# Performance work log

Hardware: AMD Instinct MI355X
Metric: run time of the kernel (lower is better)

## Reference

```python
import jax, jax.numpy as jnp
import numpy as np

N_EMBD = 1024
N_HEAD = 16
HEAD_DIM = N_EMBD // N_HEAD


def setup_inputs() -> dict:
    key = jax.random.key(0)
    kx, kq, kk, kv, ko = jax.random.split(key, 5)
    B, T, C = 2, 2048, N_EMBD
    s = 1.0 / np.sqrt(C)
    return {
        "x": jax.random.normal(kx, (B, T, C), dtype=jnp.float32),
        "Wq": jax.random.normal(kq, (C, C), dtype=jnp.float32) * s,
        "Wk": jax.random.normal(kk, (C, C), dtype=jnp.float32) * s,
        "Wv": jax.random.normal(kv, (C, C), dtype=jnp.float32) * s,
        "Wo": jax.random.normal(ko, (C, C), dtype=jnp.float32) * s,
    }


def reference(x, Wq, Wk, Wv, Wo):
    B, T, C = x.shape
    H, D = N_HEAD, HEAD_DIM
    # projections (torch Linear: y = x @ W^T)
    q = (x @ Wq.T).reshape(B, T, H, D).transpose(0, 2, 1, 3)  # [B,H,T,D]
    k = (x @ Wk.T).reshape(B, T, H, D).transpose(0, 2, 1, 3)
    v = (x @ Wv.T).reshape(B, T, H, D).transpose(0, 2, 1, 3)
    scale = 1.0 / np.sqrt(D).astype(np.float32)
    scores = jnp.einsum("bhqd,bhkd->bhqk", q, k) * scale  # [B,H,T,T]
    causal = jnp.tril(jnp.ones((T, T), dtype=bool))
    scores = jnp.where(causal, scores, -jnp.inf)
    attn = jax.nn.softmax(scores, axis=-1)
    y = jnp.einsum("bhqk,bhkd->bhqd", attn, v)  # [B,H,T,D]
    y = y.transpose(0, 2, 1, 3).reshape(B, T, C)
    return y @ Wo.T
```

## Files before the change

kernel.cpp:

```cpp
#include <hip/hip_runtime.h>
#include <hip/hip_bf16.h>
#include <math.h>

#define SEQ   2048
#define CDIM  1024
#define NH    16
#define HD    64

typedef __attribute__((ext_vector_type(8))) short bf16x8;
typedef __attribute__((ext_vector_type(4))) float f32x4;
typedef __attribute__((ext_vector_type(4))) short short4v;

__device__ __forceinline__ short f2bf(float f) {
  return (short)__builtin_bit_cast(unsigned short, __float2bfloat16(f));
}

__device__ __forceinline__ void glds16(const short* g, short* l) {
  __builtin_amdgcn_global_load_lds(
      (const __attribute__((address_space(1))) unsigned int*)g,
      (__attribute__((address_space(3))) unsigned int*)l, 16, 0, 0);
}

__global__ void cvt_kernel(const float* __restrict__ src, short* __restrict__ dst, int n4) {
  int i = blockIdx.x * blockDim.x + threadIdx.x;
  if (i >= n4) return;
  float4 v = reinterpret_cast<const float4*>(src)[i];
  short4v o;
  o.x = f2bf(v.x); o.y = f2bf(v.y); o.z = f2bf(v.z); o.w = f2bf(v.w);
  reinterpret_cast<short4v*>(dst)[i] = o;
}

template<int MODE>
__global__ __launch_bounds__(256)
void gemm_bt(const short* __restrict__ A,
             const short* __restrict__ W0, const short* __restrict__ W1, const short* __restrict__ W2,
             short* __restrict__ ob0, short* __restrict__ ob1, short* __restrict__ ob2,
             float* __restrict__ of)
{
  constexpr int K = CDIM;
  const int z = (MODE == 0) ? blockIdx.z : 0;
  const short* W;
  short* outb = nullptr;
  if (MODE == 0) {
    W    = (z == 0) ? W0  : (z == 1) ? W1  : W2;
    outb = (z == 0) ? ob0 : (z == 1) ? ob1 : ob2;
  } else {
    W = W0;
  }
  const int m0 = blockIdx.y * 128;
  const int n0 = blockIdx.x * 128;

  __shared__ __align__(16) short As[128 * 32];
  __shared__ __align__(16) short Bs[128 * 32];

  const int tid  = threadIdx.x;
  const int lane = tid & 63;
  const int wid  = tid >> 6;
  const int wr   = wid >> 1;
  const int wc   = wid & 1;
  const int rl   = lane & 15;
  const int g    = lane >> 4;

  f32x4 acc[4][4];
#pragma unroll
  for (int i = 0; i < 4; ++i)
#pragma unroll
    for (int j = 0; j < 4; ++j)
      acc[i][j] = (f32x4){0.f, 0.f, 0.f, 0.f};

  const int lrow = lane >> 2;
  const int lcol = (lane & 3) * 8;
  const int arow = wid * 32 + lrow;

  for (int kt = 0; kt < K / 32; ++kt) {
    const int k0 = kt * 32;
    glds16(&A[(size_t)(m0 + arow) * K + k0 + lcol],      &As[(wid * 32) * 32]);
    glds16(&A[(size_t)(m0 + arow + 16) * K + k0 + lcol], &As[(wid * 32 + 16) * 32]);
    glds16(&W[(size_t)(n0 + arow) * K + k0 + lcol],      &Bs[(wid * 32) * 32]);
    glds16(&W[(size_t)(n0 + arow + 16) * K + k0 + lcol], &Bs[(wid * 32 + 16) * 32]);
    __syncthreads();

    bf16x8 af[4], bfr[4];
#pragma unroll
    for (int mi = 0; mi < 4; ++mi)
      af[mi] = *(const bf16x8*)&As[(wr * 64 + mi * 16 + rl) * 32 + g * 8];
#pragma unroll
    for (int nj = 0; nj < 4; ++nj)
      bfr[nj] = *(const bf16x8*)&Bs[(wc * 64 + nj * 16 + rl) * 32 + g * 8];
#pragma unroll
    for (int mi = 0; mi < 4; ++mi)
#pragma unroll
      for (int nj = 0; nj < 4; ++nj)
        acc[mi][nj] = __builtin_amdgcn_mfma_f32_16x16x32_bf16(af[mi], bfr[nj], acc[mi][nj], 0, 0, 0);
    __syncthreads();
  }

#pragma unroll
  for (int mi = 0; mi < 4; ++mi) {
#pragma unroll
    for (int nj = 0; nj < 4; ++nj) {
      const int gmb = m0 + wr * 64 + mi * 16 + g * 4;
      const int gn  = n0 + wc * 64 + nj * 16 + rl;
      if (MODE == 0 && z == 2) {
        short4v pk;
#pragma unroll
        for (int r = 0; r < 4; ++r) pk[r] = f2bf(acc[mi][nj][r]);
        const int b = gmb >> 11, t = gmb & 2047;
        const int h = gn >> 6,  d = gn & 63;
        *(short4v*)&outb[(((size_t)(b * NH + h)) * HD + d) * SEQ + t] = pk;
      } else {
#pragma unroll
        for (int r = 0; r < 4; ++r) {
          const int gm = gmb + r;
          const float val = acc[mi][nj][r];
          if (MODE == 0) {
            const int b = gm >> 11, t = gm & 2047;
            const int h = gn >> 6,  d = gn & 63;
            outb[(((size_t)(b * NH + h)) * SEQ + t) * HD + d] = f2bf(val);
          } else {
            of[(size_t)gm * CDIM + gn] = val;
          }
        }
      }
    }
  }
}

__global__ __launch_bounds__(256)
void attn_kernel(const short* __restrict__ q, const short* __restrict__ k,
                 const short* __restrict__ vt, short* __restrict__ yb)
{
  const int bh  = blockIdx.y;
  const int pp  = blockIdx.x;
  const int jA  = pp;
  const int jB  = 31 - pp;
  const int tid = threadIdx.x;
  const int lane = tid & 63;
  const int wid  = tid >> 6;
  const int rl   = lane & 15;
  const int g    = lane >> 4;

  const short* Qp = q  + (size_t)bh * SEQ * HD;
  const short* Kp = k  + (size_t)bh * SEQ * HD;
  const short* Vp = vt + (size_t)bh * HD * SEQ;

  __shared__ short Ks[64 * 72];
  __shared__ short Vs[64 * 72];
  __shared__ short Ps[4][2][16 * 72];

  const int q0A = jA * 64 + wid * 16;
  const int q0B = jB * 64 + wid * 16;

  bf16x8 qfA[2], qfB[2];
#pragma unroll
  for (int ds = 0; ds < 2; ++ds) {
    qfA[ds] = *(const bf16x8*)&Qp[(size_t)(q0A + rl) * HD + ds * 32 + g * 8];
    qfB[ds] = *(const bf16x8*)&Qp[(size_t)(q0B + rl) * HD + ds * 32 + g * 8];
  }

  f32x4 accA[4], accB[4];
  float mA[4], lA[4], mB[4], lB[4];
#pragma unroll
  for (int r = 0; r < 4; ++r) { mA[r] = -INFINITY; lA[r] = 0.f; mB[r] = -INFINITY; lB[r] = 0.f; }
#pragma unroll
  for (int nt = 0; nt < 4; ++nt) { accA[nt] = (f32x4){0,0,0,0}; accB[nt] = (f32x4){0,0,0,0}; }

  const float scale = 0.125f;
  const int srow = tid >> 3;
  const int scol = (tid & 7) * 8;

  auto process = [&](bf16x8 (&qf)[2], f32x4 (&acc)[4], float (&m_run)[4], float (&l_run)[4],
                     bool diag, short* PsW) {
    f32x4 s_[4];
#pragma unroll
    for (int ct = 0; ct < 4; ++ct) s_[ct] = (f32x4){0, 0, 0, 0};
    __builtin_amdgcn_s_setprio(1);
#pragma unroll
    for (int ct = 0; ct < 4; ++ct)
#pragma unroll
      for (int ds = 0; ds < 2; ++ds) {
        bf16x8 kf = *(const bf16x8*)&Ks[(ct * 16 + rl) * 72 + ds * 32 + g * 8];
        s_[ct] = __builtin_amdgcn_mfma_f32_16x16x32_bf16(qf[ds], kf, s_[ct], 0, 0, 0);
      }
    __builtin_amdgcn_s_setprio(0);

    float pm[4] = {-INFINITY, -INFINITY, -INFINITY, -INFINITY};
#pragma unroll
    for (int ct = 0; ct < 4; ++ct)
#pragma unroll
      for (int r = 0; r < 4; ++r) {
        float sv = s_[ct][r] * scale;
        if (diag) {
          const int lq = wid * 16 + g * 4 + r;
          const int lk = ct * 16 + rl;
          sv = (lk <= lq) ? sv : -INFINITY;
        }
        s_[ct][r] = sv;
        pm[r] = fmaxf(pm[r], sv);
      }

    bool need = false;
#pragma unroll
    for (int r = 0; r < 4; ++r) need = need || (pm[r] > m_run[r]);
    if (__any((int)need)) {
#pragma unroll
      for (int r = 0; r < 4; ++r) {
        pm[r] = fmaxf(pm[r], __shfl_xor(pm[r], 1));
        pm[r] = fmaxf(pm[r], __shfl_xor(pm[r], 2));
        pm[r] = fmaxf(pm[r], __shfl_xor(pm[r], 4));
        pm[r] = fmaxf(pm[r], __shfl_xor(pm[r], 8));
        const float mnew = fmaxf(m_run[r], pm[r]);
        const float f = __expf(m_run[r] - mnew);
        m_run[r] = mnew;
        l_run[r] *= f;
#pragma unroll
        for (int nt = 0; nt < 4; ++nt) acc[nt][r] *= f;
      }
    }

#pragma unroll
    for (int ct = 0; ct < 4; ++ct) {
      const int c = ct * 16 + rl;
#pragma unroll
      for (int r = 0; r < 4; ++r) {
        const float p = __expf(s_[ct][r] - m_run[r]);
        l_run[r] += p;
        PsW[(g * 4 + r) * 72 + c] = f2bf(p);
      }
    }

    __builtin_amdgcn_s_setprio(1);
#pragma unroll
    for (int ks = 0; ks < 2; ++ks) {
      bf16x8 pf = *(const bf16x8*)&PsW[rl * 72 + ks * 32 + g * 8];
#pragma unroll
      for (int nt = 0; nt < 4; ++nt) {
        bf16x8 vf = *(const bf16x8*)&Vs[(nt * 16 + rl) * 72 + ks * 32 + g * 8];
        acc[nt] = __builtin_amdgcn_mfma_f32_16x16x32_bf16(pf, vf, acc[nt], 0, 0, 0);
      }
    }
    __builtin_amdgcn_s_setprio(0);
  };

  auto epilogue = [&](f32x4 (&acc)[4], float (&l_run)[4], int q0w) {
    const int b = bh >> 4, h = bh & 15;
#pragma unroll
    for (int r = 0; r < 4; ++r) {
      float lr = l_run[r];
      lr += __shfl_xor(lr, 1);
      lr += __shfl_xor(lr, 2);
      lr += __shfl_xor(lr, 4);
      lr += __shfl_xor(lr, 8);
      const float inv = 1.0f / lr;
      const int qq = q0w + g * 4 + r;
#pragma unroll
      for (int nt = 0; nt < 4; ++nt)
        yb[((size_t)b * SEQ + qq) * CDIM + h * HD + nt * 16 + rl] = f2bf(acc[nt][r] * inv);
    }
  };

  bf16x8 k0 = *(const bf16x8*)&Kp[(size_t)srow * HD + scol];
  bf16x8 k1 = *(const bf16x8*)&Kp[(size_t)(srow + 32) * HD + scol];
  bf16x8 v0 = *(const bf16x8*)&Vp[(size_t)srow * SEQ + scol];
  bf16x8 v1 = *(const bf16x8*)&Vp[(size_t)(srow + 32) * SEQ + scol];

  for (int t = 0; t <= jB; ++t) {
    __syncthreads();
    *(bf16x8*)&Ks[srow * 72 + scol]        = k0;
    *(bf16x8*)&Ks[(srow + 32) * 72 + scol] = k1;
    *(bf16x8*)&Vs[srow * 72 + scol]        = v0;
    *(bf16x8*)&Vs[(srow + 32) * 72 + scol] = v1;
    __syncthreads();

    if (t < jB) {
      const int kn = (t + 1) * 64;
      k0 = *(const bf16x8*)&Kp[(size_t)(kn + srow) * HD + scol];
      k1 = *(const bf16x8*)&Kp[(size_t)(kn + srow + 32) * HD + scol];
      v0 = *(const bf16x8*)&Vp[(size_t)srow * SEQ + kn + scol];
      v1 = *(const bf16x8*)&Vp[(size_t)(srow + 32) * SEQ + kn + scol];
    }

    process(qfB, accB, mB, lB, t == jB, &Ps[wid][0][0]);
    if (t <= jA)
      process(qfA, accA, mA, lA, t == jA, &Ps[wid][1][0]);
  }

  epilogue(accB, lB, q0B);
  epilogue(accA, lA, q0A);
}

extern "C" void kernel_launch(void* const* d_in, const int* in_sizes, int n_in,
                              void* d_out, int out_size, void* d_ws, size_t ws_size,
                              hipStream_t stream) {
  const float* x  = (const float*)d_in[0];
  const float* Wq = (const float*)d_in[1];
  const float* Wk = (const float*)d_in[2];
  const float* Wv = (const float*)d_in[3];
  const float* Wo = (const float*)d_in[4];
  float* out = (float*)d_out;

  char* ws = (char*)d_ws;
  short* xb  = (short*)(ws);
  short* Wqb = (short*)(ws + ((size_t)8  << 20));
  short* Wkb = (short*)(ws + ((size_t)10 << 20));
  short* Wvb = (short*)(ws + ((size_t)12 << 20));
  short* Wob = (short*)(ws + ((size_t)14 << 20));
  short* qb  = (short*)(ws + ((size_t)16 << 20));
  short* kbp = (short*)(ws + ((size_t)24 << 20));
  short* vtp = (short*)(ws + ((size_t)32 << 20));
  short* yb  = (short*)(ws + ((size_t)40 << 20));

  cvt_kernel<<<4096, 256, 0, stream>>>(x,  xb,  1048576);
  cvt_kernel<<<1024, 256, 0, stream>>>(Wq, Wqb, 262144);
  cvt_kernel<<<1024, 256, 0, stream>>>(Wk, Wkb, 262144);
  cvt_kernel<<<1024, 256, 0, stream>>>(Wv, Wvb, 262144);
  cvt_kernel<<<1024, 256, 0, stream>>>(Wo, Wob, 262144);

  gemm_bt<0><<<dim3(8, 32, 3), 256, 0, stream>>>(xb, Wqb, Wkb, Wvb, qb, kbp, vtp, nullptr);

  attn_kernel<<<dim3(16, 32), 256, 0, stream>>>(qb, kbp, vtp, yb);

  gemm_bt<1><<<dim3(8, 32, 1), 256, 0, stream>>>(yb, Wob, nullptr, nullptr,
                                                 nullptr, nullptr, nullptr, out);
}
```

Measured before the change: 137.8 us.

## Split attention into 32-row query tiles with per-wave pairing and exp2 softmax

The attention kernel now works on 32-row query tiles with twice as many blocks. Waves 0-1 take the late tile jB and waves 2-3 take the early tile jA, so each wave keeps one accumulator set instead of two. Causal masking uses absolute key and query indices, and the softmax uses exp2f with log2(e) folded into the scale. A launch-bounds occupancy hint of 4 is added. The aim is more parallelism and lower register pressure, at the cost of more blocks each reloading K/V, and waves 2-3 idle on later iterations while the block still loads K/V up to tile jB.

Result: slower. 149.8 us (+8.7%).

```diff
diff --git a/kernel.cpp b/kernel.cpp
--- a/kernel.cpp
+++ b/kernel.cpp
@@ -126,14 +126,14 @@
   }
 }
 
-__global__ __launch_bounds__(256)
+__global__ __launch_bounds__(256, 4)
 void attn_kernel(const short* __restrict__ q, const short* __restrict__ k,
                  const short* __restrict__ vt, short* __restrict__ yb)
 {
   const int bh  = blockIdx.y;
   const int pp  = blockIdx.x;
   const int jA  = pp;
-  const int jB  = 31 - pp;
+  const int jB  = 63 - pp;
   const int tid = threadIdx.x;
   const int lane = tid & 63;
   const int wid  = tid >> 6;
@@ -146,103 +146,127 @@
 
   __shared__ short Ks[64 * 72];
   __shared__ short Vs[64 * 72];
-  __shared__ short Ps[4][2][16 * 72];
-
-  const int q0A = jA * 64 + wid * 16;
-  const int q0B = jB * 64 + wid * 16;
-
-  bf16x8 qfA[2], qfB[2];
-#pragma unroll
-  for (int ds = 0; ds < 2; ++ds) {
-    qfA[ds] = *(const bf16x8*)&Qp[(size_t)(q0A + rl) * HD + ds * 32 + g * 8];
-    qfB[ds] = *(const bf16x8*)&Qp[(size_t)(q0B + rl) * HD + ds * 32 + g * 8];
-  }
-
-  f32x4 accA[4], accB[4];
-  float mA[4], lA[4], mB[4], lB[4];
-#pragma unroll
-  for (int r = 0; r < 4; ++r) { mA[r] = -INFINITY; lA[r] = 0.f; mB[r] = -INFINITY; lB[r] = 0.f; }
-#pragma unroll
-  for (int nt = 0; nt < 4; ++nt) { accA[nt] = (f32x4){0,0,0,0}; accB[nt] = (f32x4){0,0,0,0}; }
-
-  const float scale = 0.125f;
+  __shared__ short Ps[4][16 * 72];
+
+  const int tB    = (32 * jB + 31) >> 6;
+  const int myJ   = (wid < 2) ? jB : jA;
+  const int tLast = (32 * myJ + 31) >> 6;
+  const int q0w   = myJ * 32 + (wid & 1) * 16;
+
+  bf16x8 qf[2];
+#pragma unroll
+  for (int ds = 0; ds < 2; ++ds)
+    qf[ds] = *(const bf16x8*)&Qp[(size_t)(q0w + rl) * HD + ds * 32 + g * 8];
+
+  f32x4 acc[4];
+  float m_run[4], l_run[4];
+#pragma unroll
+  for (int r = 0; r < 4; ++r) { m_run[r] = -INFINITY; l_run[r] = 0.f; }
+#pragma unroll
+  for (int nt = 0; nt < 4; ++nt) acc[nt] = (f32x4){0, 0, 0, 0};
+
+  const float scale2 = 0.125f * 1.44269504088896340736f;
   const int srow = tid >> 3;
   const int scol = (tid & 7) * 8;
 
-  auto process = [&](bf16x8 (&qf)[2], f32x4 (&acc)[4], float (&m_run)[4], float (&l_run)[4],
-                     bool diag, short* PsW) {
-    f32x4 s_[4];
-#pragma unroll
-    for (int ct = 0; ct < 4; ++ct) s_[ct] = (f32x4){0, 0, 0, 0};
-    __builtin_amdgcn_s_setprio(1);
-#pragma unroll
-    for (int ct = 0; ct < 4; ++ct)
-#pragma unroll
-      for (int ds = 0; ds < 2; ++ds) {
-        bf16x8 kf = *(const bf16x8*)&Ks[(ct * 16 + rl) * 72 + ds * 32 + g * 8];
-        s_[ct] = __builtin_amdgcn_mfma_f32_16x16x32_bf16(qf[ds], kf, s_[ct], 0, 0, 0);
+  bf16x8 k0 = *(const bf16x8*)&Kp[(size_t)srow * HD + scol];
+  bf16x8 k1 = *(const bf16x8*)&Kp[(size_t)(srow + 32) * HD + scol];
+  bf16x8 v0 = *(const bf16x8*)&Vp[(size_t)srow * SEQ + scol];
+  bf16x8 v1 = *(const bf16x8*)&Vp[(size_t)(srow + 32) * SEQ + scol];
+
+  for (int t = 0; t <= tB; ++t) {
+    __syncthreads();
+    *(bf16x8*)&Ks[srow * 72 + scol]        = k0;
+    *(bf16x8*)&Ks[(srow + 32) * 72 + scol] = k1;
+    *(bf16x8*)&Vs[srow * 72 + scol]        = v0;
+    *(bf16x8*)&Vs[(srow + 32) * 72 + scol] = v1;
+    __syncthreads();
+
+    if (t < tB) {
+      const int kn = (t + 1) * 64;
+      k0 = *(const bf16x8*)&Kp[(size_t)(kn + srow) * HD + scol];
+      k1 = *(const bf16x8*)&Kp[(size_t)(kn + srow + 32) * HD + scol];
+      v0 = *(const bf16x8*)&Vp[(size_t)srow * SEQ + kn + scol];
+      v1 = *(const bf16x8*)&Vp[(size_t)(srow + 32) * SEQ + kn + scol];
+    }
+
+    if (t <= tLast) {
+      const bool diag = (t == tLast);
+      short* PsW = &Ps[wid][0];
+
+      f32x4 s_[4];
+#pragma unroll
+      for (int ct = 0; ct < 4; ++ct) s_[ct] = (f32x4){0, 0, 0, 0};
+      __builtin_amdgcn_s_setprio(1);
+#pragma unroll
+      for (int ct = 0; ct < 4; ++ct)
+#pragma unroll
+        for (int ds = 0; ds < 2; ++ds) {
+          bf16x8 kf = *(const bf16x8*)&Ks[(ct * 16 + rl) * 72 + ds * 32 + g * 8];
+          s_[ct] = __builtin_amdgcn_mfma_f32_16x16x32_bf16(qf[ds], kf, s_[ct], 0, 0, 0);
+        }
+      __builtin_amdgcn_s_setprio(0);
+
+      float pm[4] = {-INFINITY, -INFINITY, -INFINITY, -INFINITY};
+#pragma unroll
+      for (int ct = 0; ct < 4; ++ct)
+#pragma unroll
+        for (int r = 0; r < 4; ++r) {
+          float sv = s_[ct][r] * scale2;
+          if (diag) {
+            const int key = t * 64 + ct * 16 + rl;
+            const int qq  = q0w + g * 4 + r;
+            sv = (key <= qq) ? sv : -INFINITY;
+          }
+          s_[ct][r] = sv;
+          pm[r] = fmaxf(pm[r], sv);
+        }
+
+      bool need = false;
+#pragma unroll
+      for (int r = 0; r < 4; ++r) need = need || (pm[r] > m_run[r]);
+      if (__any((int)need)) {
+#pragma unroll
+        for (int r = 0; r < 4; ++r) {
+          pm[r] = fmaxf(pm[r], __shfl_xor(pm[r], 1));
+          pm[r] = fmaxf(pm[r], __shfl_xor(pm[r], 2));
+          pm[r] = fmaxf(pm[r], __shfl_xor(pm[r], 4));
+          pm[r] = fmaxf(pm[r], __shfl_xor(pm[r], 8));
+          const float mnew = fmaxf(m_run[r], pm[r]);
+          const float f = exp2f(m_run[r] - mnew);
+          m_run[r] = mnew;
+          l_run[r] *= f;
+#pragma unroll
+          for (int nt = 0; nt < 4; ++nt) acc[nt][r] *= f;
+        }
       }
-    __builtin_amdgcn_s_setprio(0);
-
-    float pm[4] = {-INFINITY, -INFINITY, -INFINITY, -INFINITY};
-#pragma unroll
-    for (int ct = 0; ct < 4; ++ct)
-#pragma unroll
-      for (int r = 0; r < 4; ++r) {
-        float sv = s_[ct][r] * scale;
-        if (diag) {
-          const int lq = wid * 16 + g * 4 + r;
-          const int lk = ct * 16 + rl;
-          sv = (lk <= lq) ? sv : -INFINITY;
-        }
-        s_[ct][r] = sv;
-        pm[r] = fmaxf(pm[r], sv);
+
+#pragma unroll
+      for (int ct = 0; ct < 4; ++ct) {
+        const int c = ct * 16 + rl;
+#pragma unroll
+        for (int r = 0; r < 4; ++r) {
+          const float p = exp2f(s_[ct][r] - m_run[r]);
+          l_run[r] += p;
+          PsW[(g * 4 + r) * 72 + c] = f2bf(p);
+        }
       }
 
-    bool need = false;
-#pragma unroll
-    for (int r = 0; r < 4; ++r) need = need || (pm[r] > m_run[r]);
-    if (__any((int)need)) {
-#pragma unroll
-      for (int r = 0; r < 4; ++r) {
-        pm[r] = fmaxf(pm[r], __shfl_xor(pm[r], 1));
-        pm[r] = fmaxf(pm[r], __shfl_xor(pm[r], 2));
-        pm[r] = fmaxf(pm[r], __shfl_xor(pm[r], 4));
-        pm[r] = fmaxf(pm[r], __shfl_xor(pm[r], 8));
-        const float mnew = fmaxf(m_run[r], pm[r]);
-        const float f = __expf(m_run[r] - mnew);
-        m_run[r] = mnew;
-        l_run[r] *= f;
-#pragma unroll
-        for (int nt = 0; nt < 4; ++nt) acc[nt][r] *= f;
+      __builtin_amdgcn_s_setprio(1);
+#pragma unroll
+      for (int ks = 0; ks < 2; ++ks) {
+        bf16x8 pf = *(const bf16x8*)&PsW[rl * 72 + ks * 32 + g * 8];
+#pragma unroll
+        for (int nt = 0; nt < 4; ++nt) {
+          bf16x8 vf = *(const bf16x8*)&Vs[(nt * 16 + rl) * 72 + ks * 32 + g * 8];
+          acc[nt] = __builtin_amdgcn_mfma_f32_16x16x32_bf16(pf, vf, acc[nt], 0, 0, 0);
+        }
       }
+      __builtin_amdgcn_s_setprio(0);
     }
-
-#pragma unroll
-    for (int ct = 0; ct < 4; ++ct) {
-      const int c = ct * 16 + rl;
-#pragma unroll
-      for (int r = 0; r < 4; ++r) {
-        const float p = __expf(s_[ct][r] - m_run[r]);
-        l_run[r] += p;
-        PsW[(g * 4 + r) * 72 + c] = f2bf(p);
-      }
-    }
-
-    __builtin_amdgcn_s_setprio(1);
-#pragma unroll
-    for (int ks = 0; ks < 2; ++ks) {
-      bf16x8 pf = *(const bf16x8*)&PsW[rl * 72 + ks * 32 + g * 8];
-#pragma unroll
-      for (int nt = 0; nt < 4; ++nt) {
-        bf16x8 vf = *(const bf16x8*)&Vs[(nt * 16 + rl) * 72 + ks * 32 + g * 8];
-        acc[nt] = __builtin_amdgcn_mfma_f32_16x16x32_bf16(pf, vf, acc[nt], 0, 0, 0);
-      }
-    }
-    __builtin_amdgcn_s_setprio(0);
-  };
-
-  auto epilogue = [&](f32x4 (&acc)[4], float (&l_run)[4], int q0w) {
+  }
+
+  {
     const int b = bh >> 4, h = bh & 15;
 #pragma unroll
     for (int r = 0; r < 4; ++r) {
@@ -257,36 +281,7 @@
       for (int nt = 0; nt < 4; ++nt)
         yb[((size_t)b * SEQ + qq) * CDIM + h * HD + nt * 16 + rl] = f2bf(acc[nt][r] * inv);
     }
-  };
-
-  bf16x8 k0 = *(const bf16x8*)&Kp[(size_t)srow * HD + scol];
-  bf16x8 k1 = *(const bf16x8*)&Kp[(size_t)(srow + 32) * HD + scol];
-  bf16x8 v0 = *(const bf16x8*)&Vp[(size_t)srow * SEQ + scol];
-  bf16x8 v1 = *(const bf16x8*)&Vp[(size_t)(srow + 32) * SEQ + scol];
-
-  for (int t = 0; t <= jB; ++t) {
-    __syncthreads();
-    *(bf16x8*)&Ks[srow * 72 + scol]        = k0;
-    *(bf16x8*)&Ks[(srow + 32) * 72 + scol] = k1;
-    *(bf16x8*)&Vs[srow * 72 + scol]        = v0;
-    *(bf16x8*)&Vs[(srow + 32) * 72 + scol] = v1;
-    __syncthreads();
-
-    if (t < jB) {
-      const int kn = (t + 1) * 64;
-      k0 = *(const bf16x8*)&Kp[(size_t)(kn + srow) * HD + scol];
-      k1 = *(const bf16x8*)&Kp[(size_t)(kn + srow + 32) * HD + scol];
-      v0 = *(const bf16x8*)&Vp[(size_t)srow * SEQ + kn + scol];
-      v1 = *(const bf16x8*)&Vp[(size_t)(srow + 32) * SEQ + kn + scol];
-    }
-
-    process(qfB, accB, mB, lB, t == jB, &Ps[wid][0][0]);
-    if (t <= jA)
-      process(qfA, accA, mA, lA, t == jA, &Ps[wid][1][0]);
-  }
-
-  epilogue(accB, lB, q0B);
-  epilogue(accA, lA, q0A);
+  }
 }
 
 extern "C" void kernel_launch(void* const* d_in, const int* in_sizes, int n_in,
@@ -318,7 +313,7 @@
 
   gemm_bt<0><<<dim3(8, 32, 3), 256, 0, stream>>>(xb, Wqb, Wkb, Wvb, qb, kbp, vtp, nullptr);
 
-  attn_kernel<<<dim3(16, 32), 256, 0, stream>>>(qb, kbp, vtp, yb);
+  attn_kernel<<<dim3(32, 32), 256, 0, stream>>>(qb, kbp, vtp, yb);
 
   gemm_bt<1><<<dim3(8, 32, 1), 256, 0, stream>>>(yb, Wob, nullptr, nullptr,
                                                  nullptr, nullptr, nullptr, out);
```

## Double-buffer K/V tiles and interleave paired query-tile MFMAs in attention

Applied to the files above, without the earlier changes.

Uses two LDS buffers for K and V so one barrier per iteration suffices instead of two. It also restructures the paired query tiles A and B to share each K/V fragment load, issuing their QK^T and PV MFMAs interleaved and separating the softmax into its own stage. The scale is folded into log2(e) so exp2f replaces __expf. The cost is higher LDS use and register pressure from keeping two score tiles live.

Result: slower. 151.6 us (+10.0%).

```diff
diff --git a/kernel.cpp b/kernel.cpp
--- a/kernel.cpp
+++ b/kernel.cpp
@@ -144,8 +144,8 @@
   const short* Kp = k  + (size_t)bh * SEQ * HD;
   const short* Vp = vt + (size_t)bh * HD * SEQ;
 
-  __shared__ short Ks[64 * 72];
-  __shared__ short Vs[64 * 72];
+  __shared__ short Ks[2][64 * 72];
+  __shared__ short Vs[2][64 * 72];
   __shared__ short Ps[4][2][16 * 72];
 
   const int q0A = jA * 64 + wid * 16;
@@ -165,40 +165,26 @@
 #pragma unroll
   for (int nt = 0; nt < 4; ++nt) { accA[nt] = (f32x4){0,0,0,0}; accB[nt] = (f32x4){0,0,0,0}; }
 
-  const float scale = 0.125f;
+  const float scale2 = 0.125f * 1.44269504088896340736f;
   const int srow = tid >> 3;
   const int scol = (tid & 7) * 8;
 
-  auto process = [&](bf16x8 (&qf)[2], f32x4 (&acc)[4], float (&m_run)[4], float (&l_run)[4],
-                     bool diag, short* PsW) {
-    f32x4 s_[4];
-#pragma unroll
-    for (int ct = 0; ct < 4; ++ct) s_[ct] = (f32x4){0, 0, 0, 0};
-    __builtin_amdgcn_s_setprio(1);
+  auto softmax_set = [&](f32x4 (&s_)[4], f32x4 (&acc)[4], float (&m_run)[4], float (&l_run)[4],
+                         bool diag, int t, int q0w, short* PsW) {
+    float pm[4] = {-INFINITY, -INFINITY, -INFINITY, -INFINITY};
 #pragma unroll
     for (int ct = 0; ct < 4; ++ct)
 #pragma unroll
-      for (int ds = 0; ds < 2; ++ds) {
-        bf16x8 kf = *(const bf16x8*)&Ks[(ct * 16 + rl) * 72 + ds * 32 + g * 8];
-        s_[ct] = __builtin_amdgcn_mfma_f32_16x16x32_bf16(qf[ds], kf, s_[ct], 0, 0, 0);
-      }
-    __builtin_amdgcn_s_setprio(0);
-
-    float pm[4] = {-INFINITY, -INFINITY, -INFINITY, -INFINITY};
-#pragma unroll
-    for (int ct = 0; ct < 4; ++ct)
-#pragma unroll
       for (int r = 0; r < 4; ++r) {
-        float sv = s_[ct][r] * scale;
+        float sv = s_[ct][r] * scale2;
         if (diag) {
-          const int lq = wid * 16 + g * 4 + r;
-          const int lk = ct * 16 + rl;
-          sv = (lk <= lq) ? sv : -INFINITY;
+          const int key = t * 64 + ct * 16 + rl;
+          const int qq  = q0w + g * 4 + r;
+          sv = (key <= qq) ? sv : -INFINITY;
         }
         s_[ct][r] = sv;
         pm[r] = fmaxf(pm[r], sv);
       }
-
     bool need = false;
 #pragma unroll
     for (int r = 0; r < 4; ++r) need = need || (pm[r] > m_run[r]);
@@ -210,36 +196,23 @@
         pm[r] = fmaxf(pm[r], __shfl_xor(pm[r], 4));
         pm[r] = fmaxf(pm[r], __shfl_xor(pm[r], 8));
         const float mnew = fmaxf(m_run[r], pm[r]);
-        const float f = __expf(m_run[r] - mnew);
+        const float f = exp2f(m_run[r] - mnew);
         m_run[r] = mnew;
         l_run[r] *= f;
 #pragma unroll
         for (int nt = 0; nt < 4; ++nt) acc[nt][r] *= f;
       }
     }
-
 #pragma unroll
     for (int ct = 0; ct < 4; ++ct) {
       const int c = ct * 16 + rl;
 #pragma unroll
       for (int r = 0; r < 4; ++r) {
-        const float p = __expf(s_[ct][r] - m_run[r]);
+        const float p = exp2f(s_[ct][r] - m_run[r]);
         l_run[r] += p;
         PsW[(g * 4 + r) * 72 + c] = f2bf(p);
       }
     }
-
-    __builtin_amdgcn_s_setprio(1);
-#pragma unroll
-    for (int ks = 0; ks < 2; ++ks) {
-      bf16x8 pf = *(const bf16x8*)&PsW[rl * 72 + ks * 32 + g * 8];
-#pragma unroll
-      for (int nt = 0; nt < 4; ++nt) {
-        bf16x8 vf = *(const bf16x8*)&Vs[(nt * 16 + rl) * 72 + ks * 32 + g * 8];
-        acc[nt] = __builtin_amdgcn_mfma_f32_16x16x32_bf16(pf, vf, acc[nt], 0, 0, 0);
-      }
-    }
-    __builtin_amdgcn_s_setprio(0);
   };
 
   auto epilogue = [&](f32x4 (&acc)[4], float (&l_run)[4], int q0w) {
@@ -265,11 +238,11 @@
   bf16x8 v1 = *(const bf16x8*)&Vp[(size_t)(srow + 32) * SEQ + scol];
 
   for (int t = 0; t <= jB; ++t) {
-    __syncthreads();
-    *(bf16x8*)&Ks[srow * 72 + scol]        = k0;
-    *(bf16x8*)&Ks[(srow + 32) * 72 + scol] = k1;
-    *(bf16x8*)&Vs[srow * 72 + scol]        = v0;
-    *(bf16x8*)&Vs[(srow + 32) * 72 + scol] = v1;
+    const int c = t & 1;
+    *(bf16x8*)&Ks[c][srow * 72 + scol]        = k0;
+    *(bf16x8*)&Ks[c][(srow + 32) * 72 + scol] = k1;
+    *(bf16x8*)&Vs[c][srow * 72 + scol]        = v0;
+    *(bf16x8*)&Vs[c][(srow + 32) * 72 + scol] = v1;
     __syncthreads();
 
     if (t < jB) {
@@ -280,9 +253,61 @@
       v1 = *(const bf16x8*)&Vp[(size_t)(srow + 32) * SEQ + kn + scol];
     }
 
-    process(qfB, accB, mB, lB, t == jB, &Ps[wid][0][0]);
-    if (t <= jA)
-      process(qfA, accA, mA, lA, t == jA, &Ps[wid][1][0]);
+    const bool liveA = (t <= jA);
+
+    f32x4 sB[4], sA[4];
+#pragma unroll
+    for (int ct = 0; ct < 4; ++ct) { sB[ct] = (f32x4){0,0,0,0}; sA[ct] = (f32x4){0,0,0,0}; }
+    __builtin_amdgcn_s_setprio(1);
+    if (liveA) {
+#pragma unroll
+      for (int ct = 0; ct < 4; ++ct)
+#pragma unroll
+        for (int ds = 0; ds < 2; ++ds) {
+          bf16x8 kf = *(const bf16x8*)&Ks[c][(ct * 16 + rl) * 72 + ds * 32 + g * 8];
+          sB[ct] = __builtin_amdgcn_mfma_f32_16x16x32_bf16(qfB[ds], kf, sB[ct], 0, 0, 0);
+          sA[ct] = __builtin_amdgcn_mfma_f32_16x16x32_bf16(qfA[ds], kf, sA[ct], 0, 0, 0);
+        }
+    } else {
+#pragma unroll
+      for (int ct = 0; ct < 4; ++ct)
+#pragma unroll
+        for (int ds = 0; ds < 2; ++ds) {
+          bf16x8 kf = *(const bf16x8*)&Ks[c][(ct * 16 + rl) * 72 + ds * 32 + g * 8];
+          sB[ct] = __builtin_amdgcn_mfma_f32_16x16x32_bf16(qfB[ds], kf, sB[ct], 0, 0, 0);
+        }
+    }
+    __builtin_amdgcn_s_setprio(0);
+
+    softmax_set(sB, accB, mB, lB, t == jB, t, q0B, &Ps[wid][0][0]);
+    if (liveA)
+      softmax_set(sA, accA, mA, lA, t == jA, t, q0A, &Ps[wid][1][0]);
+
+    __builtin_amdgcn_s_setprio(1);
+    if (liveA) {
+#pragma unroll
+      for (int ks = 0; ks < 2; ++ks) {
+        bf16x8 pfB = *(const bf16x8*)&Ps[wid][0][rl * 72 + ks * 32 + g * 8];
+        bf16x8 pfA = *(const bf16x8*)&Ps[wid][1][rl * 72 + ks * 32 + g * 8];
+#pragma unroll
+        for (int nt = 0; nt < 4; ++nt) {
+          bf16x8 vf = *(const bf16x8*)&Vs[c][(nt * 16 + rl) * 72 + ks * 32 + g * 8];
+          accB[nt] = __builtin_amdgcn_mfma_f32_16x16x32_bf16(pfB, vf, accB[nt], 0, 0, 0);
+          accA[nt] = __builtin_amdgcn_mfma_f32_16x16x32_bf16(pfA, vf, accA[nt], 0, 0, 0);
+        }
+      }
+    } else {
+#pragma unroll
+      for (int ks = 0; ks < 2; ++ks) {
+        bf16x8 pfB = *(const bf16x8*)&Ps[wid][0][rl * 72 + ks * 32 + g * 8];
+#pragma unroll
+        for (int nt = 0; nt < 4; ++nt) {
+          bf16x8 vf = *(const bf16x8*)&Vs[c][(nt * 16 + rl) * 72 + ks * 32 + g * 8];
+          accB[nt] = __builtin_amdgcn_mfma_f32_16x16x32_bf16(pfB, vf, accB[nt], 0, 0, 0);
+        }
+      }
+    }
+    __builtin_amdgcn_s_setprio(0);
   }
 
   epilogue(accB, lB, q0B);
```
